# Performance work log

Measured on AMD Instinct MI355X. Metric: run time of the kernel, lower is better.

## Reference

```python
import jax, jax.numpy as jnp
import numpy as np

N = 100000
E = 1600000


def gcn_conv(x, W, b, src, dst, n_nodes):
    """PyG GCNConv: linear -> add self loops -> sym-normalized scatter-add."""
    h = x @ W  # [N, out]
    # degree with self-loops: deg[i] = 1 + in_degree(i)
    deg = jax.ops.segment_sum(jnp.ones((src.shape[0],), h.dtype), dst,
                              num_segments=n_nodes) + 1.0
    dinv = jax.lax.rsqrt(deg)  # deg >= 1 always
    norm = dinv[src] * dinv[dst]  # [E]
    # neighbor messages + self-loop contribution (norm = deg^-1)
    agg = jax.ops.segment_sum(h[src] * norm[:, None], dst,
                              num_segments=n_nodes)
    return agg + h * (dinv * dinv)[:, None] + b


def setup_inputs() -> dict:
    key = jax.random.key(0)
    k1, k2, k3, k4 = jax.random.split(key, 4)
    x = jax.random.normal(k1, (N, 128), dtype=jnp.float32)
    edge_index = jax.random.randint(k2, (2, E), 0, N, dtype=jnp.int64)
    W1 = jax.random.normal(k3, (128, 64), dtype=jnp.float32) * (1.0 / np.sqrt(128))
    b1 = jnp.zeros((64,), jnp.float32)
    W2 = jax.random.normal(k4, (64, 40), dtype=jnp.float32) * (1.0 / np.sqrt(64))
    b2 = jnp.zeros((40,), jnp.float32)
    return {"x": x, "edge_index": edge_index, "W1": W1, "b1": b1,
            "W2": W2, "b2": b2}


def reference(x, edge_index, W1, b1, W2, b2):
    src, dst = edge_index[0], edge_index[1]
    h = gcn_conv(x, W1, b1, src, dst, N)
    h = jax.nn.relu(h)
    # dropout is identity in eval mode; mask_features is a no-op
    h = gcn_conv(h, W2, b2, src, dst, N)
    return jax.nn.log_softmax(h, axis=1)
```

## Files before the change

### kernel.cpp

```cpp
#include <hip/hip_runtime.h>
#include <hip/hip_fp16.h>
#include <math.h>

#define N_NODES 100000
#define N_EDGES 1600000
#define F_IN    128
#define F_HID   64
#define F_OUT   40

#define BIN_SHIFT 8
#define NBINS     392
#define BIN_CAP   5120
#define FILL_BLOCKS 512
#define GEMM1_BLOCKS ((N_NODES + 63) / 64)
#define GEMM2_BLOCKS ((N_NODES + 63) / 64)
#define AGG_BLOCKS  ((N_NODES + 15) / 16)

typedef unsigned int  uint;
typedef unsigned short ushort;
typedef __attribute__((ext_vector_type(8))) _Float16 half8;
typedef __attribute__((ext_vector_type(4))) float f32x4;

__device__ __forceinline__ uint pack2h(float a, float b) {
    __half2 h = __floats2half2_rn(a, b);
    return *(const uint*)&h;
}
__device__ __forceinline__ ushort f2h(float f) {
    return __half_as_ushort(__float2half_rn(f));
}
__device__ __forceinline__ void fma8(float* acc, uint4 hv, float w) {
    const __half2* hp = (const __half2*)&hv;
    #pragma unroll
    for (int j = 0; j < 4; ++j) {
        acc[2 * j]     = fmaf(__low2float(hp[j]),  w, acc[2 * j]);
        acc[2 * j + 1] = fmaf(__high2float(hp[j]), w, acc[2 * j + 1]);
    }
}

__global__ void prep_kernel(const float* __restrict__ W, const float* __restrict__ W2,
                            uint* __restrict__ Wt, uint* __restrict__ Wt2,
                            int* __restrict__ bcursor) {
    int tid = threadIdx.x;
    if (tid < NBINS) bcursor[tid] = tid * BIN_CAP;
    for (int i = tid; i < 4096; i += 512) {
        int c  = i >> 6;
        int kp = i & 63;
        Wt[i] = pack2h(W[(2 * kp) * F_HID + c], W[(2 * kp + 1) * F_HID + c]);
    }
    for (int i = tid; i < 1536; i += 512) {
        int c  = i >> 5;
        int kp = i & 31;
        float lo = (c < F_OUT) ? W2[(2 * kp) * F_OUT + c]     : 0.f;
        float hi = (c < F_OUT) ? W2[(2 * kp + 1) * F_OUT + c] : 0.f;
        Wt2[i] = pack2h(lo, hi);
    }
}

#define XPITCH 68
__global__ __launch_bounds__(256) void fillgemm_kernel(
        const int* __restrict__ src, const int* __restrict__ dst,
        int* __restrict__ bcursor, int* __restrict__ bins, int E,
        const float* __restrict__ x, const uint* __restrict__ Wt,
        ushort* __restrict__ h, int n) {
    __shared__ __align__(16) uint smem[2 * 64 * XPITCH];
    int tid = threadIdx.x;

    if (blockIdx.x < FILL_BLOCKS) {
        int* lcount = (int*)smem;
        int* gbase  = ((int*)smem) + NBINS;
        for (int i = tid; i < NBINS; i += 256) lcount[i] = 0;
        __syncthreads();
        int chunk = (E + FILL_BLOCKS - 1) / FILL_BLOCKS;
        int beg = blockIdx.x * chunk, end = min(E, beg + chunk);
        for (int e = beg + tid; e < end; e += 256)
            atomicAdd(&lcount[dst[e] >> BIN_SHIFT], 1);
        __syncthreads();
        for (int i = tid; i < NBINS; i += 256) {
            gbase[i] = lcount[i] ? atomicAdd(&bcursor[i], lcount[i]) : 0;
            lcount[i] = 0;
        }
        __syncthreads();
        for (int e = beg + tid; e < end; e += 256) {
            int d = dst[e];
            int b = d >> BIN_SHIFT;
            int p = atomicAdd(&lcount[b], 1);
            bins[gbase[b] + p] = src[e] | ((d & 255) << 17);
        }
        return;
    }

    uint* Xu = smem;
    uint* Wu = smem + 64 * XPITCH;
    int node0 = (blockIdx.x - FILL_BLOCKS) * 64;

    {
        int c = tid >> 2, qq = tid & 3;
        const uint4* gsrc = (const uint4*)&Wt[c * 64 + qq * 16];
        uint4* ldst = (uint4*)&Wu[c * XPITCH + qq * 16];
        #pragma unroll
        for (int j = 0; j < 4; ++j) ldst[j] = gsrc[j];
    }
    {
        int row = tid >> 2, qq = tid & 3;
        int node = node0 + row;
        uint4* ldst = (uint4*)&Xu[row * XPITCH + qq * 16];
        if (node < n) {
            const float4* gsrc = (const float4*)&x[(size_t)node * F_IN + qq * 32];
            #pragma unroll
            for (int j = 0; j < 4; ++j) {
                float4 a = gsrc[2 * j], b = gsrc[2 * j + 1];
                uint4 o;
                o.x = pack2h(a.x, a.y); o.y = pack2h(a.z, a.w);
                o.z = pack2h(b.x, b.y); o.w = pack2h(b.z, b.w);
                ldst[j] = o;
            }
        } else {
            uint4 z = make_uint4(0, 0, 0, 0);
            #pragma unroll
            for (int j = 0; j < 4; ++j) ldst[j] = z;
        }
    }
    __syncthreads();

    int wv   = tid >> 6;
    int lane = tid & 63;
    int lrow = lane & 15;
    int quad = lane >> 4;

    half8 bfrag[4][4];
    #pragma unroll
    for (int t = 0; t < 4; ++t)
        #pragma unroll
        for (int s = 0; s < 4; ++s)
            bfrag[t][s] = *(const half8*)&Wu[(t * 16 + lrow) * XPITCH + s * 16 + quad * 4];

    f32x4 acc[4];
    #pragma unroll
    for (int t = 0; t < 4; ++t) acc[t] = (f32x4){0.f, 0.f, 0.f, 0.f};

    #pragma unroll
    for (int s = 0; s < 4; ++s) {
        half8 afrag = *(const half8*)&Xu[(wv * 16 + lrow) * XPITCH + s * 16 + quad * 4];
        #pragma unroll
        for (int t = 0; t < 4; ++t)
            acc[t] = __builtin_amdgcn_mfma_f32_16x16x32_f16(afrag, bfrag[t][s], acc[t], 0, 0, 0);
    }

    #pragma unroll
    for (int t = 0; t < 4; ++t) {
        #pragma unroll
        for (int i = 0; i < 4; ++i) {
            int node = node0 + wv * 16 + quad * 4 + i;
            if (node < n) h[(size_t)node * F_HID + t * 16 + lrow] = f2h(acc[t][i]);
        }
    }
}

__global__ void binsort_kernel(const int* __restrict__ bcursor, const int* __restrict__ bins,
                               int* __restrict__ csr, int* __restrict__ rowstart,
                               int* __restrict__ rowcnt, float* __restrict__ dinv) {
    __shared__ int hist[256];
    __shared__ int scan[256];
    __shared__ int cur[256];
    __shared__ int sorted[BIN_CAP];
    int b = blockIdx.x, t = threadIdx.x;
    int base = b * BIN_CAP;
    int cnt = bcursor[b] - base;
    if (t < 256) hist[t] = 0;
    __syncthreads();
    for (int i = t; i < cnt; i += 512)
        atomicAdd(&hist[(unsigned)bins[base + i] >> 17], 1);
    __syncthreads();
    int v = 0;
    if (t < 256) { v = hist[t]; scan[t] = v; }
    __syncthreads();
    for (int off = 1; off < 256; off <<= 1) {
        int u = (t < 256 && t >= off) ? scan[t - off] : 0;
        __syncthreads();
        if (t < 256) scan[t] += u;
        __syncthreads();
    }
    if (t < 256) {
        int excl = scan[t] - v;
        cur[t] = excl;
        int node = (b << BIN_SHIFT) + t;
        if (node < N_NODES) {
            rowstart[node] = base + excl;
            rowcnt[node]   = v;
            dinv[node] = rsqrtf((float)v + 1.0f);
        }
    }
    __syncthreads();
    for (int i = t; i < cnt; i += 512) {
        int p   = bins[base + i];
        int pos = atomicAdd(&cur[(unsigned)p >> 17], 1);
        sorted[pos] = p & 0x1FFFF;
    }
    __syncthreads();
    for (int i = t; i < cnt; i += 512)
        csr[base + i] = sorted[i];
}

__global__ void pack_kernel(const int* __restrict__ bcursor, const float* __restrict__ dinv,
                            int* __restrict__ csr) {
    int b = blockIdx.x, t = threadIdx.x;
    int base = b * BIN_CAP;
    int cnt = bcursor[b] - base;
    for (int i = t; i < cnt; i += 256) {
        int sid = csr[base + i] & 0x1FFFF;
        uint hb = (uint)__half_as_ushort(__float2half_rn(dinv[sid]));
        csr[base + i] = sid | (int)(hb << 17);
    }
}

__device__ __forceinline__ float wgt_of(uint e) {
    return __half2float(__ushort_as_half((ushort)(e >> 17)));
}

__global__ void agg1_kernel(const int* __restrict__ rowstart, const int* __restrict__ rowcnt,
                            const int* __restrict__ csr, const float* __restrict__ dinv,
                            const ushort* __restrict__ h, const float* __restrict__ b,
                            ushort* __restrict__ out, int n) {
    int lane = threadIdx.x & 63;
    int sub  = lane >> 4;
    int l16  = lane & 15;
    int slot = l16 >> 3;
    int c    = l16 & 7;
    int node = blockIdx.x * 16 + (threadIdx.x >> 6) * 4 + sub;
    if (node >= n) return;
    int beg = rowstart[node], end = beg + rowcnt[node];
    int lbase = (lane & 48) + slot;
    float acc[8] = {0.f,0.f,0.f,0.f,0.f,0.f,0.f,0.f};
    for (int base = beg; base < end; base += 16) {
        int idx = base + l16;
        int   sid = 0; float wgt = 0.f;
        if (idx < end) { uint e = (uint)csr[idx]; sid = e & 0x1FFFF; wgt = wgt_of(e); }
        int   sa[8]; float w[8];
        #pragma unroll
        for (int g = 0; g < 8; ++g) {
            sa[g] = __shfl(sid, lbase + 2 * g);
            w[g]  = __shfl(wgt, lbase + 2 * g);
        }
        uint4 hv[8];
        #pragma unroll
        for (int g = 0; g < 8; ++g)
            hv[g] = *(const uint4*)&h[(size_t)sa[g] * F_HID + (c << 3)];
        #pragma unroll
        for (int g = 0; g < 8; ++g) fma8(acc, hv[g], w[g]);
    }
    #pragma unroll
    for (int k = 0; k < 8; ++k) acc[k] += __shfl_xor(acc[k], 8);
    if (slot == 0) {
        float di  = dinv[node];
        float di2 = di * di;
        uint4 hs = *(const uint4*)&h[(size_t)node * F_HID + (c << 3)];
        const __half2* hp = (const __half2*)&hs;
        float4 b0  = *(const float4*)&b[c << 3];
        float4 b1v = *(const float4*)&b[(c << 3) + 4];
        float bb[8] = { b0.x, b0.y, b0.z, b0.w, b1v.x, b1v.y, b1v.z, b1v.w };
        float v[8];
        #pragma unroll
        for (int k = 0; k < 4; ++k) {
            v[2*k]   = fmaxf(fmaf(acc[2*k],   di, __low2float(hp[k])  * di2) + bb[2*k],   0.f);
            v[2*k+1] = fmaxf(fmaf(acc[2*k+1], di, __high2float(hp[k]) * di2) + bb[2*k+1], 0.f);
        }
        uint4 pk;
        pk.x = pack2h(v[0], v[1]); pk.y = pack2h(v[2], v[3]);
        pk.z = pack2h(v[4], v[5]); pk.w = pack2h(v[6], v[7]);
        *(uint4*)&out[(size_t)node * F_HID + (c << 3)] = pk;
    }
}

__global__ __launch_bounds__(256) void gemm2_kernel(const ushort* __restrict__ a,
        const uint* __restrict__ Wt2, ushort* __restrict__ lo, ushort* __restrict__ hi,
        int n) {
    int tid  = threadIdx.x;
    int wv   = tid >> 6;
    int lane = tid & 63;
    int lrow = lane & 15;
    int quad = lane >> 4;
    int node0 = blockIdx.x * 64;
    const uint* au = (const uint*)a;

    half8 bfrag[3][2];
    #pragma unroll
    for (int t = 0; t < 3; ++t)
        #pragma unroll
        for (int s = 0; s < 2; ++s)
            bfrag[t][s] = *(const half8*)&Wt2[(t * 16 + lrow) * 32 + s * 16 + quad * 4];

    f32x4 acc[3];
    #pragma unroll
    for (int t = 0; t < 3; ++t) acc[t] = (f32x4){0.f, 0.f, 0.f, 0.f};

    int arow = node0 + wv * 16 + lrow;
    #pragma unroll
    for (int s = 0; s < 2; ++s) {
        half8 afrag = *(const half8*)&au[(size_t)arow * 32 + s * 16 + quad * 4];
        #pragma unroll
        for (int t = 0; t < 3; ++t)
            acc[t] = __builtin_amdgcn_mfma_f32_16x16x32_f16(afrag, bfrag[t][s], acc[t], 0, 0, 0);
    }

    #pragma unroll
    for (int t = 0; t < 2; ++t) {
        #pragma unroll
        for (int i = 0; i < 4; ++i) {
            int node = node0 + wv * 16 + quad * 4 + i;
            if (node < n) lo[(size_t)node * 32 + t * 16 + lrow] = f2h(acc[t][i]);
        }
    }
    if (lrow < 8) {
        #pragma unroll
        for (int i = 0; i < 4; ++i) {
            int node = node0 + wv * 16 + quad * 4 + i;
            if (node < n) hi[(size_t)node * 8 + lrow] = f2h(acc[2][i]);
        }
    }
}

__global__ void agg2_kernel(const int* __restrict__ rowstart, const int* __restrict__ rowcnt,
                            const int* __restrict__ csr, const float* __restrict__ dinv,
                            const ushort* __restrict__ lo, const ushort* __restrict__ hi,
                            const float* __restrict__ b, float* __restrict__ out, int n) {
    int lane = threadIdx.x & 63;
    int sub  = lane >> 4;
    int l16  = lane & 15;
    int slot = l16 >> 3;
    int c    = l16 & 7;
    int node = blockIdx.x * 16 + (threadIdx.x >> 6) * 4 + sub;
    if (node >= n) return;
    int beg = rowstart[node], end = beg + rowcnt[node];
    int lbase = (lane & 48) + slot;
    float acc[8] = {0.f,0.f,0.f,0.f,0.f,0.f,0.f,0.f};
    for (int base = beg; base < end; base += 16) {
        int idx = base + l16;
        int   sid = 0; float wgt = 0.f;
        if (idx < end) { uint e = (uint)csr[idx]; sid = e & 0x1FFFF; wgt = wgt_of(e); }
        int   sa[8]; float w[8];
        #pragma unroll
        for (int g = 0; g < 8; ++g) {
            sa[g] = __shfl(sid, lbase + 2 * g);
            w[g]  = __shfl(wgt, lbase + 2 * g);
        }
        if (c < 4) {
            uint4 hv[8];
            #pragma unroll
            for (int g = 0; g < 8; ++g)
                hv[g] = *(const uint4*)&lo[(size_t)sa[g] * 32 + (c << 3)];
            #pragma unroll
            for (int g = 0; g < 8; ++g) fma8(acc, hv[g], w[g]);
        } else if (c == 4) {
            uint4 hv[8];
            #pragma unroll
            for (int g = 0; g < 8; ++g)
                hv[g] = *(const uint4*)&hi[(size_t)sa[g] * 8];
            #pragma unroll
            for (int g = 0; g < 8; ++g) fma8(acc, hv[g], w[g]);
        }
    }
    #pragma unroll
    for (int k = 0; k < 8; ++k) acc[k] += __shfl_xor(acc[k], 8);
    bool active = (slot == 0) && (c < 5);
    float val[8];
    float mx = -INFINITY;
    if (active) {
        float di  = dinv[node];
        float di2 = di * di;
        uint4 hs = (c < 4) ? *(const uint4*)&lo[(size_t)node * 32 + (c << 3)]
                           : *(const uint4*)&hi[(size_t)node * 8];
        const __half2* hp = (const __half2*)&hs;
        float4 b0  = *(const float4*)&b[c << 3];
        float4 b1v = *(const float4*)&b[(c << 3) + 4];
        float bb[8] = { b0.x, b0.y, b0.z, b0.w, b1v.x, b1v.y, b1v.z, b1v.w };
        #pragma unroll
        for (int k = 0; k < 4; ++k) {
            val[2*k]   = fmaf(acc[2*k],   di, __low2float(hp[k])  * di2) + bb[2*k];
            val[2*k+1] = fmaf(acc[2*k+1], di, __high2float(hp[k]) * di2) + bb[2*k+1];
        }
        #pragma unroll
        for (int k = 0; k < 8; ++k) mx = fmaxf(mx, val[k]);
    }
    #pragma unroll
    for (int off = 1; off < 8; off <<= 1) mx = fmaxf(mx, __shfl_xor(mx, off));
    float p = 0.f;
    if (active) {
        #pragma unroll
        for (int k = 0; k < 8; ++k) p += __expf(val[k] - mx);
    }
    #pragma unroll
    for (int off = 1; off < 8; off <<= 1) p += __shfl_xor(p, off);
    float lse = mx + __logf(p);
    if (active) {
        float4 o0, o1;
        o0.x = val[0] - lse; o0.y = val[1] - lse; o0.z = val[2] - lse; o0.w = val[3] - lse;
        o1.x = val[4] - lse; o1.y = val[5] - lse; o1.z = val[6] - lse; o1.w = val[7] - lse;
        float* orow = &out[(size_t)node * F_OUT + (c << 3)];
        *(float4*)orow       = o0;
        *(float4*)(orow + 4) = o1;
    }
}

extern "C" void kernel_launch(void* const* d_in, const int* in_sizes, int n_in,
                              void* d_out, int out_size, void* d_ws, size_t ws_size,
                              hipStream_t stream) {
    const float* x  = (const float*)d_in[0];
    const int*   ei = (const int*)d_in[1];
    const float* W1 = (const float*)d_in[2];
    const float* b1 = (const float*)d_in[3];
    const float* W2 = (const float*)d_in[4];
    const float* b2 = (const float*)d_in[5];
    const int* src = ei;
    const int* dst = ei + N_EDGES;

    char* p = (char*)d_ws;
    int*    bcursor  = (int*)p;     p += (size_t)(NBINS + 8) * 4;
    int*    bins     = (int*)p;     p += (size_t)NBINS * BIN_CAP * 4;
    int*    csr_src  = (int*)p;     p += (size_t)NBINS * BIN_CAP * 4;
    int*    rowstart = (int*)p;     p += (size_t)(N_NODES + 4) * 4;
    int*    rowcnt   = (int*)p;     p += (size_t)(N_NODES + 4) * 4;
    float*  dinv     = (float*)p;   p += (size_t)N_NODES * 4;
    uint*   Wtb      = (uint*)p;    p += (size_t)4096 * 4;
    uint*   Wt2b     = (uint*)p;    p += (size_t)1536 * 4;
    ushort* h1b      = (ushort*)p;  p += (size_t)N_NODES * F_HID * 2;
    ushort* out1b    = (ushort*)p;  p += (size_t)N_NODES * F_HID * 2;
    ushort* h2lo     = (ushort*)p;  p += (size_t)N_NODES * 32 * 2;
    ushort* h2hi     = (ushort*)p;  p += ((size_t)N_NODES * 8 + 64) * 2;
    float*  out      = (float*)d_out;

    prep_kernel    <<<1, 512, 0, stream>>>(W1, W2, Wtb, Wt2b, bcursor);
    fillgemm_kernel<<<FILL_BLOCKS + GEMM1_BLOCKS, 256, 0, stream>>>(
        src, dst, bcursor, bins, N_EDGES, x, Wtb, h1b, N_NODES);
    binsort_kernel <<<NBINS, 512, 0, stream>>>(bcursor, bins, csr_src, rowstart, rowcnt, dinv);
    pack_kernel    <<<NBINS, 256, 0, stream>>>(bcursor, dinv, csr_src);
    agg1_kernel    <<<AGG_BLOCKS, 256, 0, stream>>>(rowstart, rowcnt, csr_src, dinv,
                                                    h1b, b1, out1b, N_NODES);
    gemm2_kernel   <<<GEMM2_BLOCKS, 256, 0, stream>>>(out1b, Wt2b, h2lo, h2hi, N_NODES);
    agg2_kernel    <<<AGG_BLOCKS, 256, 0, stream>>>(rowstart, rowcnt, csr_src, dinv,
                                                    h2lo, h2hi, b2, out, N_NODES);
}
```

Measured before the change: 256.7 us.

## Split layer-1 hidden features into column slabs for cache-local aggregation

```diff
diff --git a/kernel.cpp b/kernel.cpp
--- a/kernel.cpp
+++ b/kernel.cpp
@@ -15,6 +15,7 @@
 #define GEMM1_BLOCKS ((N_NODES + 63) / 64)
 #define GEMM2_BLOCKS ((N_NODES + 63) / 64)
 #define AGG_BLOCKS  ((N_NODES + 15) / 16)
+#define AGG1_GRID   (((AGG_BLOCKS + 1) / 2) * 8)
 
 typedef unsigned int  uint;
 typedef unsigned short ushort;
@@ -151,7 +152,8 @@
         #pragma unroll
         for (int i = 0; i < 4; ++i) {
             int node = node0 + wv * 16 + quad * 4 + i;
-            if (node < n) h[(size_t)node * F_HID + t * 16 + lrow] = f2h(acc[t][i]);
+            if (node < n)
+                h[(size_t)t * n * 16 + (size_t)node * 16 + lrow] = f2h(acc[t][i]);
         }
     }
 }
@@ -221,42 +223,47 @@
                             const int* __restrict__ csr, const float* __restrict__ dinv,
                             const ushort* __restrict__ h, const float* __restrict__ b,
                             ushort* __restrict__ out, int n) {
+    int idx8 = blockIdx.x & 7;
+    int slab = idx8 >> 1;
+    int nodeblock = (blockIdx.x >> 3) * 2 + (idx8 & 1);
+    if (nodeblock >= (n + 15) / 16) return;
     int lane = threadIdx.x & 63;
     int sub  = lane >> 4;
     int l16  = lane & 15;
-    int slot = l16 >> 3;
-    int c    = l16 & 7;
-    int node = blockIdx.x * 16 + (threadIdx.x >> 6) * 4 + sub;
+    int slot = l16 >> 1;
+    int c    = l16 & 1;
+    int node = nodeblock * 16 + (threadIdx.x >> 6) * 4 + sub;
     if (node >= n) return;
+    const ushort* hs = h + (size_t)slab * n * 16;
     int beg = rowstart[node], end = beg + rowcnt[node];
-    int lbase = (lane & 48) + slot;
+    int grp = lane & 48;
     float acc[8] = {0.f,0.f,0.f,0.f,0.f,0.f,0.f,0.f};
     for (int base = beg; base < end; base += 16) {
         int idx = base + l16;
         int   sid = 0; float wgt = 0.f;
         if (idx < end) { uint e = (uint)csr[idx]; sid = e & 0x1FFFF; wgt = wgt_of(e); }
-        int   sa[8]; float w[8];
-        #pragma unroll
-        for (int g = 0; g < 8; ++g) {
-            sa[g] = __shfl(sid, lbase + 2 * g);
-            w[g]  = __shfl(wgt, lbase + 2 * g);
-        }
-        uint4 hv[8];
-        #pragma unroll
-        for (int g = 0; g < 8; ++g)
-            hv[g] = *(const uint4*)&h[(size_t)sa[g] * F_HID + (c << 3)];
-        #pragma unroll
-        for (int g = 0; g < 8; ++g) fma8(acc, hv[g], w[g]);
-    }
-    #pragma unroll
-    for (int k = 0; k < 8; ++k) acc[k] += __shfl_xor(acc[k], 8);
-    if (slot == 0) {
+        int   sA = __shfl(sid, grp + 2 * slot);
+        float wA = __shfl(wgt, grp + 2 * slot);
+        int   sB = __shfl(sid, grp + 2 * slot + 1);
+        float wB = __shfl(wgt, grp + 2 * slot + 1);
+        uint4 hA = *(const uint4*)&hs[(size_t)sA * 16 + (c << 3)];
+        uint4 hB = *(const uint4*)&hs[(size_t)sB * 16 + (c << 3)];
+        fma8(acc, hA, wA);
+        fma8(acc, hB, wB);
+    }
+    #pragma unroll
+    for (int m = 2; m < 16; m <<= 1) {
+        #pragma unroll
+        for (int k = 0; k < 8; ++k) acc[k] += __shfl_xor(acc[k], m);
+    }
+    if (l16 < 2) {
         float di  = dinv[node];
         float di2 = di * di;
-        uint4 hs = *(const uint4*)&h[(size_t)node * F_HID + (c << 3)];
-        const __half2* hp = (const __half2*)&hs;
-        float4 b0  = *(const float4*)&b[c << 3];
-        float4 b1v = *(const float4*)&b[(c << 3) + 4];
+        uint4 hsv = *(const uint4*)&hs[(size_t)node * 16 + (l16 << 3)];
+        const __half2* hp = (const __half2*)&hsv;
+        int fb = slab * 16 + (l16 << 3);
+        float4 b0  = *(const float4*)&b[fb];
+        float4 b1v = *(const float4*)&b[fb + 4];
         float bb[8] = { b0.x, b0.y, b0.z, b0.w, b1v.x, b1v.y, b1v.z, b1v.w };
         float v[8];
         #pragma unroll
@@ -267,7 +274,7 @@
         uint4 pk;
         pk.x = pack2h(v[0], v[1]); pk.y = pack2h(v[2], v[3]);
         pk.z = pack2h(v[4], v[5]); pk.w = pack2h(v[6], v[7]);
-        *(uint4*)&out[(size_t)node * F_HID + (c << 3)] = pk;
+        *(uint4*)&out[(size_t)node * F_HID + fb] = pk;
     }
 }
 
@@ -433,8 +440,8 @@
         src, dst, bcursor, bins, N_EDGES, x, Wtb, h1b, N_NODES);
     binsort_kernel <<<NBINS, 512, 0, stream>>>(bcursor, bins, csr_src, rowstart, rowcnt, dinv);
     pack_kernel    <<<NBINS, 256, 0, stream>>>(bcursor, dinv, csr_src);
-    agg1_kernel    <<<AGG_BLOCKS, 256, 0, stream>>>(rowstart, rowcnt, csr_src, dinv,
-                                                    h1b, b1, out1b, N_NODES);
+    agg1_kernel    <<<AGG1_GRID, 256, 0, stream>>>(rowstart, rowcnt, csr_src, dinv,
+                                                   h1b, b1, out1b, N_NODES);
     gemm2_kernel   <<<GEMM2_BLOCKS, 256, 0, stream>>>(out1b, Wt2b, h2lo, h2hi, N_NODES);
     agg2_kernel    <<<AGG_BLOCKS, 256, 0, stream>>>(rowstart, rowcnt, csr_src, dinv,
                                                     h2lo, h2hi, b2, out, N_NODES);
```

New measurement: 265.0 us. 1.03x slower.
